# Performance work log

Measured on AMD Instinct MI355X. Metric: run time of the kernel, lower is better.

The kernel has to match this reference:

```python
import jax, jax.numpy as jnp
import numpy as np

K = 3      # kernel_size
PAD = 1    # padding


def setup_inputs() -> dict:
    key = jax.random.key(0)
    ks = jax.random.split(key, 5)
    B, Cin, Cout, H, W = 8, 64, 64, 128, 128
    x = jax.random.normal(ks[0], (B, Cin, H, W), jnp.float32)
    # offset conv params (zero-init in the module; use small random values so the
    # deformable gather path is actually exercised)
    offset_w = jax.random.normal(ks[1], (2 * K, Cin, K, K), jnp.float32) * 0.01
    offset_b = jax.random.normal(ks[2], (2 * K,), jnp.float32) * 0.01
    # kaiming-normal strip weights
    std = float(np.sqrt(2.0 / (Cin * K)))
    w_h = jax.random.normal(ks[3], (Cout, Cin, 1, K), jnp.float32) * std
    w_v = jax.random.normal(ks[4], (Cout, Cin, K, 1), jnp.float32) * std
    return {"x": x, "offset_w": offset_w, "offset_b": offset_b, "w_h": w_h, "w_v": w_v}


def _bilinear_gather(x, py, px):
    # x: [B,C,H,W]; py, px: [B,K,H,W] float sampling coordinates.
    # Returns bilinearly sampled values [B,C,K,H,W] with zero padding outside.
    B, C, H, W = x.shape
    y0 = jnp.floor(py)
    x0 = jnp.floor(px)
    wy1 = py - y0
    wx1 = px - x0

    def corner(yf, xf, w):
        valid = ((yf >= 0) & (yf <= H - 1) & (xf >= 0) & (xf <= W - 1)).astype(x.dtype)
        yi = jnp.clip(yf, 0, H - 1).astype(jnp.int32)
        xi = jnp.clip(xf, 0, W - 1).astype(jnp.int32)
        v = jax.vmap(lambda im, yy, xx: im[:, yy, xx])(x, yi, xi)  # [B,C,K,H,W]
        return v * (w * valid)[:, None]

    return (corner(y0, x0, (1 - wy1) * (1 - wx1))
            + corner(y0, x0 + 1, (1 - wy1) * wx1)
            + corner(y0 + 1, x0, wy1 * (1 - wx1))
            + corner(y0 + 1, x0 + 1, wy1 * wx1))


def reference(x, offset_w, offset_b, w_h, w_v):
    B, C, H, W = x.shape
    # offset conv (standard 3x3, stride 1, pad 1) -> [B, 2K, H, W]
    off = jax.lax.conv_general_dilated(
        x, offset_w, window_strides=(1, 1), padding=((PAD, PAD), (PAD, PAD)),
        dimension_numbers=("NCHW", "OIHW", "NCHW")) + offset_b[None, :, None, None]
    h_off = off[:, :K]   # per-tap vertical (y) offsets for the horizontal strip
    v_off = off[:, K:]   # per-tap horizontal (x) offsets for the vertical strip

    ygrid = jnp.arange(H, dtype=x.dtype)
    xgrid = jnp.arange(W, dtype=x.dtype)
    taps = jnp.arange(K, dtype=x.dtype) - PAD  # tap displacements along the strip

    # horizontal strip: taps move along x, deform offsets bend the strip in y
    py_h = ygrid[None, None, :, None] + h_off                              # [B,K,H,W]
    px_h = jnp.broadcast_to(xgrid[None, None, None, :] + taps[None, :, None, None],
                            (B, K, H, W))
    val_h = _bilinear_gather(x, py_h, px_h)                                # [B,C,K,H,W]
    out_h = jnp.einsum("bckhw,ock->bohw", val_h, w_h[:, :, 0, :])

    # vertical strip: taps move along y, deform offsets bend the strip in x
    py_v = jnp.broadcast_to(ygrid[None, None, :, None] + taps[None, :, None, None],
                            (B, K, H, W))
    px_v = xgrid[None, None, None, :] + v_off
    val_v = _bilinear_gather(x, py_v, px_v)
    out_v = jnp.einsum("bckhw,ock->bohw", val_v, w_v[:, :, :, 0])

    return out_h + out_v
```

## Files before the change

### kernel.cpp

```cpp
#include <hip/hip_runtime.h>

#define HH 128
#define WW 128
#define HW (HH * WW)
#define CIN 64
#define COUT 64

#define XT_OFF  0
#define BF_OFF  16777216
#define OBF_OFF (BF_OFF + 49152)

typedef short bf16x8 __attribute__((ext_vector_type(8)));
typedef float f32x4 __attribute__((ext_vector_type(4)));

__device__ __forceinline__ unsigned short f2bf(float f) {
    union { float f; unsigned int u; } v; v.f = f;
    unsigned int r = v.u + 0x7FFFu + ((v.u >> 16) & 1u);
    return (unsigned short)(r >> 16);
}
__device__ __forceinline__ unsigned short f2bf_up(float f) {
    union { float f; unsigned int u; } v; v.f = f;
    return (unsigned short)((v.u + 0x8000u) >> 16);
}
__device__ __forceinline__ float bf2f(unsigned short u) {
    union { unsigned int u; float f; } v; v.u = ((unsigned int)u) << 16;
    return v.f;
}

__global__ __launch_bounds__(256) void prep_repack_kernel(const float* __restrict__ x,
                                                          const float* __restrict__ ow,
                                                          const float* __restrict__ wh,
                                                          const float* __restrict__ wv,
                                                          unsigned short* __restrict__ xT,
                                                          unsigned short* __restrict__ Bf,
                                                          unsigned short* __restrict__ OBf) {
    __shared__ float tile[64 * 129];
    const int tid = threadIdx.x;
    const int blk = blockIdx.x;

    if (blk < 1024) {
        const int b = blk & 7;
        const int y = blk >> 3;
        const float* xb = x + (size_t)b * CIN * HW + y * WW;
        const int tx = tid & 127;
        const int th = tid >> 7;
        for (int c0 = 0; c0 < 64; c0 += 2) {
            int c = c0 + th;
            tile[c * 129 + tx] = xb[(size_t)c * HW + tx];
        }
        __syncthreads();
        unsigned short* ob = xT + ((size_t)b * HW + y * WW) * 64;
#pragma unroll
        for (int it = 0; it < 4; ++it) {
            int e  = it * 256 + tid;
            int h  = e & 7;
            int px = e >> 3;
            union { unsigned short us[8]; uint4 u4; } pkd;
#pragma unroll
            for (int j = 0; j < 8; ++j)
                pkd.us[j] = f2bf(tile[(h * 8 + j) * 129 + px]);
            *(uint4*)&ob[px * 64 + h * 8] = pkd.u4;
        }
    } else {
        int i = (blk - 1024) * 256 + tid;
        if (i < 24576) {
            int j    = i & 7;
            int lane = (i >> 3) & 63;
            int nt   = (i >> 9) & 3;
            int kc   = (i >> 11) & 1;
            int pk   = i >> 12;
            int o = nt * 16 + (lane & 15);
            int c = kc * 32 + (lane >> 4) * 8 + j;
            int k = pk % 3;
            const float* src = (pk < 3) ? wh : wv;
            Bf[i] = f2bf(src[(o * CIN + c) * 3 + k]);
        } else if (i < 24576 + 9216) {
            int mI   = i - 24576;
            int j    = mI & 7;
            int lane = (mI >> 3) & 63;
            int s    = mI >> 9;
            int n    = lane & 15;
            int q    = lane >> 4;
            int c    = (s & 1) * 32 + q * 8 + j;
            int tap  = s >> 1;
            int dy   = tap / 3, dx = tap % 3;
            OBf[mI] = (n < 6) ? f2bf(ow[((n * CIN + c) * 3 + dy) * 3 + dx])
                              : (unsigned short)0;
        }
    }
}

__global__ __launch_bounds__(256, 6) void fused_kernel(const unsigned short* __restrict__ xT,
                                                       const float* __restrict__ obias,
                                                       const unsigned short* __restrict__ Bf,
                                                       const unsigned short* __restrict__ OBf,
                                                       float* __restrict__ out) {
    __shared__ float offT[4 * 16 * 8];

    const int tid  = threadIdx.x;
    const int w    = tid >> 6;
    const int lane = tid & 63;
    const int q    = lane >> 4;
    const int m    = lane & 15;

    const int blk = blockIdx.x;
    const int b   = blk & 7;
    const int y   = (blk >> 3) & 127;
    const int xh  = blk >> 10;
    const int x0w = (xh << 6) + (w << 4);

    const unsigned short* xtb = xT + (size_t)b * HW * 64;

    f32x4 acc6 = {0.f, 0.f, 0.f, 0.f};
#pragma unroll
    for (int s = 0; s < 18; ++s) {
        const int tap  = s >> 1;
        const int dy   = tap / 3 - 1;
        const int dx   = tap % 3 - 1;
        const int coff = (s & 1) * 32 + q * 8;
        int yy = y + dy;
        int xx = x0w + m + dx;
        bool ok = (yy >= 0) && (yy < HH) && (xx >= 0) && (xx < WW);
        int yc = min(max(yy, 0), HH - 1);
        int xc = min(max(xx, 0), WW - 1);
        uint4 raw = *(const uint4*)&xtb[(size_t)(yc * WW + xc) * 64 + coff];
        if (!ok) raw = make_uint4(0, 0, 0, 0);
        union { uint4 u4; bf16x8 v; } af; af.u4 = raw;
        bf16x8 bfr = *(const bf16x8*)&OBf[(s * 64 + lane) * 8];
        acc6 = __builtin_amdgcn_mfma_f32_16x16x32_bf16(af.v, bfr, acc6, 0, 0, 0);
    }
    if (m < 6) {
        float bias = obias[m];
#pragma unroll
        for (int reg = 0; reg < 4; ++reg)
            offT[(w * 16 + q * 4 + reg) * 8 + m] = acc6[reg] + bias;
    }
    __syncthreads();
    f32x4  o03 = *(const f32x4*)&offT[(w * 16 + m) * 8];
    float2 o45 = *(const float2*)&offT[(w * 16 + m) * 8 + 4];
    float offs[6] = {o03[0], o03[1], o03[2], o03[3], o45.x, o45.y};

    const int xs = x0w + m;
    float wA[6], wB[6];
    int   iA[6], iB[6];
#pragma unroll
    for (int pk = 0; pk < 6; ++pk) {
        const int ph = pk / 3;
        const int k  = pk % 3;
        float o1 = offs[pk];
        if (ph == 0) {
            float py  = (float)y + o1;
            float y0f = floorf(py);
            float wy  = py - y0f;
            int   yi  = (int)y0f;
            bool v0 = (yi >= 0) && (yi <= HH - 1);
            bool v1 = (yi + 1 >= 0) && (yi + 1 <= HH - 1);
            int  pxx = xs + k - 1;
            bool pv  = (pxx >= 0) && (pxx <= WW - 1);
            wA[pk] = (pv && v0) ? (1.f - wy) : 0.f;
            wB[pk] = (pv && v1) ? wy : 0.f;
            int ra = min(max(yi, 0), HH - 1);
            int rb = min(max(yi + 1, 0), HH - 1);
            int ca = min(max(pxx, 0), WW - 1);
            iA[pk] = ra * WW + ca;
            iB[pk] = rb * WW + ca;
        } else {
            float pxf = (float)xs + o1;
            float x0f = floorf(pxf);
            float wx  = pxf - x0f;
            int   xi  = (int)x0f;
            bool v0 = (xi >= 0) && (xi <= WW - 1);
            bool v1 = (xi + 1 >= 0) && (xi + 1 <= WW - 1);
            int  py = y + k - 1;
            bool pv = (py >= 0) && (py <= HH - 1);
            wA[pk] = (pv && v0) ? (1.f - wx) : 0.f;
            wB[pk] = (pv && v1) ? wx : 0.f;
            int ra  = min(max(py, 0), HH - 1);
            int ca  = min(max(xi, 0), WW - 1);
            int cb2 = min(max(xi + 1, 0), WW - 1);
            iA[pk] = ra * WW + ca;
            iB[pk] = ra * WW + cb2;
        }
    }

    f32x4 acc[4];
#pragma unroll
    for (int nt = 0; nt < 4; ++nt) acc[nt] = (f32x4){0.f, 0.f, 0.f, 0.f};

#pragma unroll
    for (int pk = 0; pk < 6; ++pk) {
#pragma unroll
        for (int kc = 0; kc < 2; ++kc) {
            const int coff = kc * 32 + q * 8;
            union { uint4 u4; unsigned short us[8]; } ua, ub;
            ua.u4 = *(const uint4*)&xtb[(size_t)iA[pk] * 64 + coff];
            ub.u4 = *(const uint4*)&xtb[(size_t)iB[pk] * 64 + coff];
            union { unsigned short us[8]; bf16x8 v; } uf;
#pragma unroll
            for (int j = 0; j < 8; ++j) {
                float v = wA[pk] * bf2f(ua.us[j]) + wB[pk] * bf2f(ub.us[j]);
                uf.us[j] = f2bf_up(v);
            }
#pragma unroll
            for (int nt = 0; nt < 4; ++nt) {
                bf16x8 bfr = *(const bf16x8*)&Bf[(((pk * 2 + kc) * 4 + nt) * 64 + lane) * 8];
                acc[nt] = __builtin_amdgcn_mfma_f32_16x16x32_bf16(uf.v, bfr, acc[nt], 0, 0, 0);
            }
        }
    }

#pragma unroll
    for (int nt = 0; nt < 4; ++nt) {
        int o = nt * 16 + m;
        float* op = out + ((size_t)(b * COUT + o) * HH + y) * WW + x0w + q * 4;
        *(f32x4*)op = acc[nt];
    }
}

extern "C" void kernel_launch(void* const* d_in, const int* in_sizes, int n_in,
                              void* d_out, int out_size, void* d_ws, size_t ws_size,
                              hipStream_t stream) {
    const float* x     = (const float*)d_in[0];
    const float* ow    = (const float*)d_in[1];
    const float* obias = (const float*)d_in[2];
    const float* wh    = (const float*)d_in[3];
    const float* wv    = (const float*)d_in[4];
    float* out = (float*)d_out;

    char* ws = (char*)d_ws;
    unsigned short* xT  = (unsigned short*)(ws + XT_OFF);
    unsigned short* Bf  = (unsigned short*)(ws + BF_OFF);
    unsigned short* OBf = (unsigned short*)(ws + OBF_OFF);

    prep_repack_kernel<<<dim3(1156), dim3(256), 0, stream>>>(x, ow, wh, wv, xT, Bf, OBf);
    fused_kernel<<<dim3(2048), dim3(256), 0, stream>>>(xT, obias, Bf, OBf, out);
}
```

Measured before the change: 143.4 us.

## Stage main weights in LDS and batch gather loads ahead of MFMA loops

Copies the 48KB packed strip-conv weight fragments into shared memory at block start and reads them from LDS in the MFMA loop instead of global memory. Issues all offset-conv tap loads for each channel half, and all bilinear corner loads, up front into register arrays before computing, so more memory requests are in flight per wave. Lowers the occupancy hint from 6 to 3 blocks per CU to fit the larger LDS and register footprint. The per-block weight copy adds global traffic and a dependency, and lower occupancy may reduce latency hiding.

Result: faster. 137.7 us (-3.9%).

```diff
diff --git a/kernel.cpp b/kernel.cpp
--- a/kernel.cpp
+++ b/kernel.cpp
@@ -90,11 +90,12 @@
     }
 }
 
-__global__ __launch_bounds__(256, 6) void fused_kernel(const unsigned short* __restrict__ xT,
+__global__ __launch_bounds__(256, 3) void fused_kernel(const unsigned short* __restrict__ xT,
                                                        const float* __restrict__ obias,
                                                        const unsigned short* __restrict__ Bf,
                                                        const unsigned short* __restrict__ OBf,
                                                        float* __restrict__ out) {
+    __shared__ unsigned short BfL[24576];
     __shared__ float offT[4 * 16 * 8];
 
     const int tid  = threadIdx.x;
@@ -111,23 +112,33 @@
 
     const unsigned short* xtb = xT + (size_t)b * HW * 64;
 
+#pragma unroll
+    for (int i = 0; i < 12; ++i)
+        *(uint4*)&BfL[(i * 256 + tid) * 8] = ((const uint4*)Bf)[i * 256 + tid];
+
     f32x4 acc6 = {0.f, 0.f, 0.f, 0.f};
 #pragma unroll
-    for (int s = 0; s < 18; ++s) {
-        const int tap  = s >> 1;
-        const int dy   = tap / 3 - 1;
-        const int dx   = tap % 3 - 1;
-        const int coff = (s & 1) * 32 + q * 8;
-        int yy = y + dy;
-        int xx = x0w + m + dx;
-        bool ok = (yy >= 0) && (yy < HH) && (xx >= 0) && (xx < WW);
-        int yc = min(max(yy, 0), HH - 1);
-        int xc = min(max(xx, 0), WW - 1);
-        uint4 raw = *(const uint4*)&xtb[(size_t)(yc * WW + xc) * 64 + coff];
-        if (!ok) raw = make_uint4(0, 0, 0, 0);
-        union { uint4 u4; bf16x8 v; } af; af.u4 = raw;
-        bf16x8 bfr = *(const bf16x8*)&OBf[(s * 64 + lane) * 8];
-        acc6 = __builtin_amdgcn_mfma_f32_16x16x32_bf16(af.v, bfr, acc6, 0, 0, 0);
+    for (int half = 0; half < 2; ++half) {
+        const int coff = half * 32 + q * 8;
+        uint4 r1[9];
+        bool  okt[9];
+#pragma unroll
+        for (int tap = 0; tap < 9; ++tap) {
+            int dy = tap / 3 - 1, dx = tap % 3 - 1;
+            int yy = y + dy;
+            int xx = x0w + m + dx;
+            okt[tap] = (yy >= 0) && (yy < HH) && (xx >= 0) && (xx < WW);
+            int yc = min(max(yy, 0), HH - 1);
+            int xc = min(max(xx, 0), WW - 1);
+            r1[tap] = *(const uint4*)&xtb[(size_t)(yc * WW + xc) * 64 + coff];
+        }
+#pragma unroll
+        for (int tap = 0; tap < 9; ++tap) {
+            uint4 raw = okt[tap] ? r1[tap] : make_uint4(0, 0, 0, 0);
+            union { uint4 u4; bf16x8 v; } af; af.u4 = raw;
+            bf16x8 bfr = *(const bf16x8*)&OBf[((tap * 2 + half) * 64 + lane) * 8];
+            acc6 = __builtin_amdgcn_mfma_f32_16x16x32_bf16(af.v, bfr, acc6, 0, 0, 0);
+        }
     }
     if (m < 6) {
         float bias = obias[m];
@@ -183,18 +194,29 @@
         }
     }
 
-    f32x4 acc[4];
-#pragma unroll
-    for (int nt = 0; nt < 4; ++nt) acc[nt] = (f32x4){0.f, 0.f, 0.f, 0.f};
-
+    uint4 rA[12], rB[12];
 #pragma unroll
     for (int pk = 0; pk < 6; ++pk) {
 #pragma unroll
         for (int kc = 0; kc < 2; ++kc) {
             const int coff = kc * 32 + q * 8;
+            rA[pk * 2 + kc] = *(const uint4*)&xtb[(size_t)iA[pk] * 64 + coff];
+            rB[pk * 2 + kc] = *(const uint4*)&xtb[(size_t)iB[pk] * 64 + coff];
+        }
+    }
+
+    f32x4 acc[4];
+#pragma unroll
+    for (int nt = 0; nt < 4; ++nt) acc[nt] = (f32x4){0.f, 0.f, 0.f, 0.f};
+
+#pragma unroll
+    for (int pk = 0; pk < 6; ++pk) {
+#pragma unroll
+        for (int kc = 0; kc < 2; ++kc) {
+            const int g = pk * 2 + kc;
             union { uint4 u4; unsigned short us[8]; } ua, ub;
-            ua.u4 = *(const uint4*)&xtb[(size_t)iA[pk] * 64 + coff];
-            ub.u4 = *(const uint4*)&xtb[(size_t)iB[pk] * 64 + coff];
+            ua.u4 = rA[g];
+            ub.u4 = rB[g];
             union { unsigned short us[8]; bf16x8 v; } uf;
 #pragma unroll
             for (int j = 0; j < 8; ++j) {
@@ -203,7 +225,7 @@
             }
 #pragma unroll
             for (int nt = 0; nt < 4; ++nt) {
-                bf16x8 bfr = *(const bf16x8*)&Bf[(((pk * 2 + kc) * 4 + nt) * 64 + lane) * 8];
+                bf16x8 bfr = *(const bf16x8*)&BfL[((g * 4 + nt) * 64 + lane) * 8];
                 acc[nt] = __builtin_amdgcn_mfma_f32_16x16x32_bf16(uf.v, bfr, acc[nt], 0, 0, 0);
             }
         }
```
